# Performance work log

Hardware: AMD Instinct MI355X
Metric: run time of the kernel (lower is better)

The kernel has to match this reference:

```python
import jax, jax.numpy as jnp
import numpy as np

B, H, S, D = 2, 16, 2048, 64

def setup_inputs() -> dict:
    key = jax.random.key(0)
    kq, kk, kv = jax.random.split(key, 3)
    q = jax.random.normal(kq, (B, H, S, D), dtype=jnp.float32)
    k = jax.random.normal(kk, (B, H, S, D), dtype=jnp.float32)
    v = jax.random.normal(kv, (B, H, S, D), dtype=jnp.float32)
    return {"q": q, "k": k, "v": v}

def reference(q, k, v):
    # Faithful to the source: raw exp (no max-subtraction), no 1/sqrt(d) scaling.
    scores = jnp.einsum("bhsd,bhtd->bhst", q, k)          # [B,H,S,S]
    scores_exp = jnp.exp(scores)
    probs = scores_exp / jnp.sum(scores_exp, axis=-1, keepdims=True)
    return jnp.einsum("bhst,bhtd->bhsd", probs, v)         # [B,H,S,D]
```

## Files before the change

### kernel.cpp

```cpp
#include <hip/hip_runtime.h>


#define LOG2E 1.44269504088896340736f

typedef _Float16 half8 __attribute__((ext_vector_type(8)));
typedef _Float16 half2v __attribute__((ext_vector_type(2)));
typedef __fp16 fp16x2 __attribute__((ext_vector_type(2)));
typedef float f32x16 __attribute__((ext_vector_type(16)));

#define BH   32
#define SEQ  2048
#define DIM  64
#define QBLK 128
#define KVB  32
#define NIT  (SEQ / (2 * KVB))

union SMem {
  struct { _Float16 K[3][2][KVB * DIM]; _Float16 Vt[3][2][DIM * KVB]; } s;
  struct { float ob[2][2][2][16 * 64]; float ml[2][2][2][64]; } c;
};

static __device__ __forceinline__ unsigned pk2(float a, float b) {
  fp16x2 h = __builtin_amdgcn_cvt_pkrtz(a, b);
  return __builtin_bit_cast(unsigned, h);
}

static __device__ __forceinline__ void plswap(unsigned& a, unsigned& b) {
  asm volatile("v_permlane32_swap_b32 %0, %1" : "+v"(a), "+v"(b));
}

static __device__ __forceinline__ float xmax32(float x) {
  return fmaxf(x, __shfl_xor(x, 32));
}
static __device__ __forceinline__ float xsum32(float x) {
  return x + __shfl_xor(x, 32);
}

static __device__ __forceinline__ float dot2(unsigned a, float acc) {
  const half2v ones = {(_Float16)1.0f, (_Float16)1.0f};
  return __builtin_amdgcn_fdot2(__builtin_bit_cast(half2v, a), ones, acc, false);
}

__launch_bounds__(256, 2)
__global__ void attn_fwd(const float* __restrict__ Q, const float* __restrict__ K,
                         const float* __restrict__ V, float* __restrict__ O) {
  __shared__ __align__(16) SMem sm;

  const int tid  = threadIdx.x;
  const int lane = tid & 63;
  const int wave = tid >> 6;
  const int wq   = wave & 1;
  const int wk   = wave >> 1;
  const int hi   = lane >> 5;
  const int lq   = lane & 31;

  const int bid  = blockIdx.x;
  const int xcd  = bid & 7;
  const int slot = bid >> 3;
  const int bh   = xcd + 8 * (slot >> 4);
  const int qt   = slot & 15;

  const size_t base = (size_t)bh * SEQ * DIM;
  const int qr0 = qt * QBLK + wq * 64 + lq;
  const float* qpA = Q + base + (size_t)qr0 * DIM;
  const float* qpB = qpA + 32 * DIM;

  half8 qfA[4], qfB[4];
#pragma unroll
  for (int c = 0; c < 4; ++c) {
    float4 a0 = *(const float4*)(qpA + 16 * c + 8 * hi);
    float4 a1 = *(const float4*)(qpA + 16 * c + 8 * hi + 4);
    union { unsigned u[4]; half8 v; } h;
    h.u[0] = pk2(a0.x, a0.y); h.u[1] = pk2(a0.z, a0.w);
    h.u[2] = pk2(a1.x, a1.y); h.u[3] = pk2(a1.z, a1.w);
    qfA[c] = h.v;
    float4 b0 = *(const float4*)(qpB + 16 * c + 8 * hi);
    float4 b1 = *(const float4*)(qpB + 16 * c + 8 * hi + 4);
    h.u[0] = pk2(b0.x, b0.y); h.u[1] = pk2(b0.z, b0.w);
    h.u[2] = pk2(b1.x, b1.y); h.u[3] = pk2(b1.z, b1.w);
    qfB[c] = h.v;
  }

  f32x16 oA0 = {}, oA1 = {}, oB0 = {}, oB1 = {};
  float mA = -1e30f, lA = 0.f, mB = -1e30f, lB = 0.f;

  float4 kreg[2][2];
  float  vreg[2][8];
  const int kr  = tid >> 3;
  const int kd  = (tid & 7) * 8;
  const int vd  = tid & 63;
  const int vk0 = (tid >> 6) * 8;
  const float* kbp = K + base;
  const float* vbp = V + base;

  auto LOADT = [&](int it) {
#pragma unroll
    for (int p = 0; p < 2; ++p) {
      const int t = 2 * it + p;
      const float* kp = kbp + (size_t)(t * KVB + kr) * DIM + kd;
      kreg[p][0] = *(const float4*)(kp);
      kreg[p][1] = *(const float4*)(kp + 4);
      const float* vp = vbp + (size_t)(t * KVB + vk0) * DIM + vd;
#pragma unroll
      for (int j = 0; j < 8; ++j) vreg[p][j] = vp[j * DIM];
    }
  };

  auto STORET = [&](int b) {
#pragma unroll
    for (int p = 0; p < 2; ++p) {
      union { unsigned u[4]; half8 v; } h;
      h.u[0] = pk2(kreg[p][0].x, kreg[p][0].y);
      h.u[1] = pk2(kreg[p][0].z, kreg[p][0].w);
      h.u[2] = pk2(kreg[p][1].x, kreg[p][1].y);
      h.u[3] = pk2(kreg[p][1].z, kreg[p][1].w);
      const int idx = (kr * DIM + kd) ^ ((kr & 7) << 3);
      *(half8*)&sm.s.K[b][p][idx] = h.v;
      union { unsigned u[4]; half8 v; } g;
      g.u[0] = pk2(vreg[p][0], vreg[p][1]);
      g.u[1] = pk2(vreg[p][2], vreg[p][3]);
      g.u[2] = pk2(vreg[p][4], vreg[p][5]);
      g.u[3] = pk2(vreg[p][6], vreg[p][7]);
      const int vidx = (vd * KVB + vk0) ^ ((vd & 7) << 3);
      *(half8*)&sm.s.Vt[b][p][vidx] = g.v;
    }
  };

  auto softmax_set = [&](const f32x16& s, float& m, float& l,
                         f32x16& o0, f32x16& o1, half8& pv0, half8& pv1) {
    float t0 = fmaxf(fmaxf(s[0],  s[1]),  s[2]);
    float t1 = fmaxf(fmaxf(s[3],  s[4]),  s[5]);
    float t2 = fmaxf(fmaxf(s[6],  s[7]),  s[8]);
    float t3 = fmaxf(fmaxf(s[9],  s[10]), s[11]);
    float t4 = fmaxf(fmaxf(s[12], s[13]), s[14]);
    float t5 = fmaxf(fmaxf(t0, t1), t2);
    float t6 = fmaxf(fmaxf(t3, t4), s[15]);
    float t  = xmax32(fmaxf(t5, t6));
    if (__any(t > m + 10.f)) {
      const float mn = fmaxf(m, t);
      const float corr = __builtin_amdgcn_exp2f((m - mn) * LOG2E);
      m = mn; l *= corr;
#pragma unroll
      for (int i = 0; i < 16; ++i) { o0[i] *= corr; o1[i] *= corr; }
    }
    const float nml2 = -m * LOG2E;
    float p[16];
#pragma unroll
    for (int i = 0; i < 16; ++i)
      p[i] = __builtin_amdgcn_exp2f(__builtin_fmaf(s[i], LOG2E, nml2));

    unsigned w[8];
#pragma unroll
    for (int i = 0; i < 8; ++i) w[i] = pk2(p[2 * i], p[2 * i + 1]);

    float la = dot2(w[0], 0.f), lb2 = dot2(w[1], 0.f);
    la = dot2(w[2], la); lb2 = dot2(w[3], lb2);
    la = dot2(w[4], la); lb2 = dot2(w[5], lb2);
    la = dot2(w[6], la); lb2 = dot2(w[7], lb2);
    l += la + lb2;

    plswap(w[0], w[2]); plswap(w[1], w[3]);
    plswap(w[4], w[6]); plswap(w[5], w[7]);
    union { unsigned u[4]; half8 v; } f;
    f.u[0] = w[0]; f.u[1] = w[1]; f.u[2] = w[2]; f.u[3] = w[3];
    pv0 = f.v;
    f.u[0] = w[4]; f.u[1] = w[5]; f.u[2] = w[6]; f.u[3] = w[7];
    pv1 = f.v;
  };

  auto PVT = [&](int b, const half8& pA0, const half8& pA1,
                 const half8& pB0, const half8& pB1) {
    const _Float16* Vt = sm.s.Vt[b][wk];
    const int d0 = lq, d1 = 32 + lq;
    const int sz0 = (d0 & 7) << 3, sz1 = (d1 & 7) << 3;
    {
      half8 a = *(const half8*)&Vt[(d0 * KVB + 0 + hi * 8) ^ sz0];
      oA0 = __builtin_amdgcn_mfma_f32_32x32x16_f16(a, pA0, oA0, 0, 0, 0);
      oB0 = __builtin_amdgcn_mfma_f32_32x32x16_f16(a, pB0, oB0, 0, 0, 0);
    }
    {
      half8 a = *(const half8*)&Vt[(d1 * KVB + 0 + hi * 8) ^ sz1];
      oA1 = __builtin_amdgcn_mfma_f32_32x32x16_f16(a, pA0, oA1, 0, 0, 0);
      oB1 = __builtin_amdgcn_mfma_f32_32x32x16_f16(a, pB0, oB1, 0, 0, 0);
    }
    {
      half8 a = *(const half8*)&Vt[(d0 * KVB + 16 + hi * 8) ^ sz0];
      oA0 = __builtin_amdgcn_mfma_f32_32x32x16_f16(a, pA1, oA0, 0, 0, 0);
      oB0 = __builtin_amdgcn_mfma_f32_32x32x16_f16(a, pB1, oB0, 0, 0, 0);
    }
    {
      half8 a = *(const half8*)&Vt[(d1 * KVB + 16 + hi * 8) ^ sz1];
      oA1 = __builtin_amdgcn_mfma_f32_32x32x16_f16(a, pA1, oA1, 0, 0, 0);
      oB1 = __builtin_amdgcn_mfma_f32_32x32x16_f16(a, pB1, oB1, 0, 0, 0);
    }
  };

  LOADT(0);
  STORET(0);
  LOADT(1);
  __syncthreads();

  half8 pA0, pA1, pB0, pB1;

  for (int it = 0; it < NIT; ++it) {
    const _Float16* Kt = sm.s.K[it % 3][wk];
    const int ksw = (lq & 7) << 3;
    f32x16 sA = {}, sB = {};
#pragma unroll
    for (int c = 0; c < 4; ++c) {
      half8 a = *(const half8*)&Kt[(lq * DIM + c * 16 + hi * 8) ^ ksw];
      sA = __builtin_amdgcn_mfma_f32_32x32x16_f16(a, qfA[c], sA, 0, 0, 0);
      sB = __builtin_amdgcn_mfma_f32_32x32x16_f16(a, qfB[c], sB, 0, 0, 0);
    }

    if (it > 0) PVT((it + 2) % 3, pA0, pA1, pB0, pB1);

    softmax_set(sA, mA, lA, oA0, oA1, pA0, pA1);
    softmax_set(sB, mB, lB, oB0, oB1, pB0, pB1);

    if (it + 1 < NIT) {
      STORET((it + 1) % 3);
      if (it + 2 < NIT) LOADT(it + 2);
    }
    __syncthreads();
  }

  PVT((NIT - 1) % 3, pA0, pA1, pB0, pB1);

  lA = xsum32(lA);
  lB = xsum32(lB);

  __syncthreads();
  if (wk == 1) {
#pragma unroll
    for (int r = 0; r < 16; ++r) {
      sm.c.ob[wq][0][0][r * 64 + lane] = oA0[r];
      sm.c.ob[wq][0][1][r * 64 + lane] = oA1[r];
      sm.c.ob[wq][1][0][r * 64 + lane] = oB0[r];
      sm.c.ob[wq][1][1][r * 64 + lane] = oB1[r];
    }
    sm.c.ml[wq][0][0][lane] = mA; sm.c.ml[wq][0][1][lane] = lA;
    sm.c.ml[wq][1][0][lane] = mB; sm.c.ml[wq][1][1][lane] = lB;
  }
  __syncthreads();
  if (wk == 0) {
    auto emit = [&](int set, int qrow, const f32x16& o0, const f32x16& o1,
                    float m, float l) {
      const float mb = sm.c.ml[wq][set][0][lane];
      const float lb = sm.c.ml[wq][set][1][lane];
      const float mx = fmaxf(m, mb);
      const float ca = __builtin_amdgcn_exp2f((m - mx) * LOG2E);
      const float cb = __builtin_amdgcn_exp2f((mb - mx) * LOG2E);
      const float inv = 1.0f / (l * ca + lb * cb);
      float* op = O + base + (size_t)qrow * DIM;
#pragma unroll
      for (int g = 0; g < 4; ++g) {
        float4 r0, r1;
        r0.x = (o0[4*g+0] * ca + sm.c.ob[wq][set][0][(4*g+0)*64 + lane] * cb) * inv;
        r0.y = (o0[4*g+1] * ca + sm.c.ob[wq][set][0][(4*g+1)*64 + lane] * cb) * inv;
        r0.z = (o0[4*g+2] * ca + sm.c.ob[wq][set][0][(4*g+2)*64 + lane] * cb) * inv;
        r0.w = (o0[4*g+3] * ca + sm.c.ob[wq][set][0][(4*g+3)*64 + lane] * cb) * inv;
        r1.x = (o1[4*g+0] * ca + sm.c.ob[wq][set][1][(4*g+0)*64 + lane] * cb) * inv;
        r1.y = (o1[4*g+1] * ca + sm.c.ob[wq][set][1][(4*g+1)*64 + lane] * cb) * inv;
        r1.z = (o1[4*g+2] * ca + sm.c.ob[wq][set][1][(4*g+2)*64 + lane] * cb) * inv;
        r1.w = (o1[4*g+3] * ca + sm.c.ob[wq][set][1][(4*g+3)*64 + lane] * cb) * inv;
        *(float4*)(op + 8 * g + 4 * hi) = r0;
        *(float4*)(op + 32 + 8 * g + 4 * hi) = r1;
      }
    };
    emit(0, qr0,      oA0, oA1, mA, lA);
    emit(1, qr0 + 32, oB0, oB1, mB, lB);
  }
}

extern "C" void kernel_launch(void* const* d_in, const int* in_sizes, int n_in,
                              void* d_out, int out_size, void* d_ws, size_t ws_size,
                              hipStream_t stream) {
  const float* q = (const float*)d_in[0];
  const float* k = (const float*)d_in[1];
  const float* v = (const float*)d_in[2];
  float* o = (float*)d_out;
  attn_fwd<<<BH * (SEQ / QBLK), 256, 0, stream>>>(q, k, v, o);
}
```

Measured before the change: 63.43 us.

## Process two KV tiles per iteration with a four-stage LDS ring buffer

```diff
diff --git a/kernel.cpp b/kernel.cpp
--- a/kernel.cpp
+++ b/kernel.cpp
@@ -16,7 +16,7 @@
 #define NIT  (SEQ / (2 * KVB))
 
 union SMem {
-  struct { _Float16 K[3][2][KVB * DIM]; _Float16 Vt[3][2][DIM * KVB]; } s;
+  struct { _Float16 K[4][2][KVB * DIM]; _Float16 Vt[4][2][DIM * KVB]; } s;
   struct { float ob[2][2][2][16 * 64]; float ml[2][2][2][64]; } c;
 };
 
@@ -126,6 +126,18 @@
     }
   };
 
+  auto QKT = [&](int b, f32x16& sA, f32x16& sB) {
+    const _Float16* Kt = sm.s.K[b][wk];
+    const int ksw = (lq & 7) << 3;
+    sA = {}; sB = {};
+#pragma unroll
+    for (int c = 0; c < 4; ++c) {
+      half8 a = *(const half8*)&Kt[(lq * DIM + c * 16 + hi * 8) ^ ksw];
+      sA = __builtin_amdgcn_mfma_f32_32x32x16_f16(a, qfA[c], sA, 0, 0, 0);
+      sB = __builtin_amdgcn_mfma_f32_32x32x16_f16(a, qfB[c], sB, 0, 0, 0);
+    }
+  };
+
   auto softmax_set = [&](const f32x16& s, float& m, float& l,
                          f32x16& o0, f32x16& o1, half8& pv0, half8& pv1) {
     float t0 = fmaxf(fmaxf(s[0],  s[1]),  s[2]);
@@ -198,39 +210,43 @@
   LOADT(0);
   STORET(0);
   LOADT(1);
+  STORET(1);
+  LOADT(2);
   __syncthreads();
 
-  half8 pA0, pA1, pB0, pB1;
-
-  for (int it = 0; it < NIT; ++it) {
-    const _Float16* Kt = sm.s.K[it % 3][wk];
-    const int ksw = (lq & 7) << 3;
-    f32x16 sA = {}, sB = {};
-#pragma unroll
-    for (int c = 0; c < 4; ++c) {
-      half8 a = *(const half8*)&Kt[(lq * DIM + c * 16 + hi * 8) ^ ksw];
-      sA = __builtin_amdgcn_mfma_f32_32x32x16_f16(a, qfA[c], sA, 0, 0, 0);
-      sB = __builtin_amdgcn_mfma_f32_32x32x16_f16(a, qfB[c], sB, 0, 0, 0);
-    }
-
-    if (it > 0) PVT((it + 2) % 3, pA0, pA1, pB0, pB1);
-
-    softmax_set(sA, mA, lA, oA0, oA1, pA0, pA1);
-    softmax_set(sB, mB, lB, oB0, oB1, pB0, pB1);
-
-    if (it + 1 < NIT) {
-      STORET((it + 1) % 3);
-      if (it + 2 < NIT) LOADT(it + 2);
-    }
+  for (int j = 0; j < NIT / 2; ++j) {
+    const int t = 2 * j;
+    const int bA = t & 3, bB = (t + 1) & 3;
+
+    if (t + 2 < NIT) {
+      STORET((t + 2) & 3);
+      LOADT(t + 3);
+    }
+
+    f32x16 sA0, sB0, sA1, sB1;
+    QKT(bA, sA0, sB0);
+    QKT(bB, sA1, sB1);
+
+    half8 pA0, pA1, pB0, pB1;
+    softmax_set(sA0, mA, lA, oA0, oA1, pA0, pA1);
+    softmax_set(sB0, mB, lB, oB0, oB1, pB0, pB1);
+    PVT(bA, pA0, pA1, pB0, pB1);
+
+    if (t + 3 < NIT) {
+      STORET((t + 3) & 3);
+      if (t + 4 < NIT) LOADT(t + 4);
+    }
+
+    softmax_set(sA1, mA, lA, oA0, oA1, pA0, pA1);
+    softmax_set(sB1, mB, lB, oB0, oB1, pB0, pB1);
+    PVT(bB, pA0, pA1, pB0, pB1);
+
     __syncthreads();
   }
 
-  PVT((NIT - 1) % 3, pA0, pA1, pB0, pB1);
-
   lA = xsum32(lA);
   lB = xsum32(lB);
 
-  __syncthreads();
   if (wk == 1) {
 #pragma unroll
     for (int r = 0; r < 16; ++r) {
```

New measurement: 61.96 us, median of 2. 2.3% less time.
